# Optimization experiments

Hardware: AMD Instinct MI355X
Metric: run time of the kernel (lower is better)

## Reference

```python
import jax, jax.numpy as jnp
import numpy as np

N_HEADS = 8


def _norm_weights(idx):
    # softmax over where(idx>0, 1, -9e15) along axis 1 -> uniform weights over non-pad slots
    logits = jnp.where(idx > 0, jnp.float32(1.0), jnp.float32(-9e15))
    return jax.nn.softmax(logits, axis=1)


def _layer_norm(x, g, b, eps=1e-6):
    mu = jnp.mean(x, axis=-1, keepdims=True)
    var = jnp.var(x, axis=-1, keepdims=True)
    return (x - mu) * jax.lax.rsqrt(var + eps) * g + b


def _mha_block(x, mask, wq, wk, wv, wo, g, b):
    # standard multi-head self-attention block with residual + layernorm
    B, L, D = x.shape
    hd = D // N_HEADS
    q = (x @ wq).reshape(B, L, N_HEADS, hd)
    k = (x @ wk).reshape(B, L, N_HEADS, hd)
    v = (x @ wv).reshape(B, L, N_HEADS, hd)
    scores = jnp.einsum('bqhd,bkhd->bhqk', q, k) / jnp.float32(np.sqrt(hd))
    scores = jnp.where(mask[:, None, None, :], jnp.float32(-1e9), scores)
    attn = jax.nn.softmax(scores, axis=-1)
    out = jnp.einsum('bhqk,bkhd->bqhd', attn, v).reshape(B, L, D) @ wo
    return _layer_norm(out + x, g, b)


def _forward(data_idx, seq, timestamps, user_level, useq, user_inf, user_cen,
             spread_status, id2vector,
             user_emb, cen_emb, time_emb, pos_emb, inf_emb,
             w1, w2, w3,
             t_wq, t_wk, t_wv, t_wo, t_g, t_b,
             s_wq, s_wk, s_wv, s_wo, s_g, s_b,
             W, W2, f_l1_w, f_l1_b, f_l2_w, f_l2_b, lin_w, lin_b):
    # ---- HGNN layer (hypergraph conv) ----
    tv = w3[0]  # TextVector = weight3[0]
    dot = w3 @ tv
    cos = dot / (jnp.linalg.norm(tv) * jnp.linalg.norm(w3, axis=1))
    inter_nw = jnp.mean(cos)  # scalar

    tweet_hidden = user_emb + cen_emb[user_cen]          # [N, D]
    x = (tweet_hidden @ w1) * inter_nw                   # [N, D]
    nor = _norm_weights(seq)                             # [E, L]
    edge = jnp.einsum('elc,el->ec', x[seq], nor)         # gather + weighted reduce
    edge = jax.nn.relu(edge)
    e1 = edge @ w2                                       # [E, D]
    u_nor = _norm_weights(useq)                          # [N, Lu]
    node = jnp.einsum('nlc,nl->nc', e1[useq], u_nor)     # [N, D]

    # ---- HGSL head ----
    sb = seq[data_idx]                                   # [B, L]
    nor_b = _norm_weights(sb)
    att_mask = sb == 0                                   # PAD == 0
    adj = node[sb]                                       # [B, L, D]

    att_hidden = adj + time_emb[timestamps[data_idx]]
    att_out = _mha_block(att_hidden, att_mask, t_wq, t_wk, t_wv, t_wo, t_g, t_b)
    news = jnp.einsum('blc,bl->bc', att_out, nor_b)
    news = jnp.concatenate([news, spread_status[data_idx][:, 2:] / 3600.0 / 24.0], axis=-1) @ W

    att_hidden_s = adj + inf_emb[user_inf[data_idx]] + pos_emb[user_level[data_idx]]
    att_out_s = _mha_block(att_hidden_s, att_mask, s_wq, s_wk, s_wv, s_wo, s_g, s_b)
    news_s = jnp.einsum('blc,bl->bc', att_out_s, nor_b)
    news_s = jnp.concatenate([news_s, spread_status[data_idx][:, :2]], axis=-1) @ W2

    # Gated fusion (linear3 unused in original forward; id2vector is overwritten/unused)
    emb = jnp.stack([news, news_s], axis=0)              # [2, B, D+2]
    score = jax.nn.softmax(jnp.tanh(emb @ f_l1_w + f_l1_b) @ f_l2_w + f_l2_b, axis=0)
    fused = jnp.sum(score * emb, axis=0)                 # [B, D+2]
    return jax.nn.log_softmax(fused @ lin_w + lin_b, axis=1)


def setup_inputs():
    key = jax.random.key(0)
    ks = jax.random.split(key, 40)
    N, E, L, Lu, D, B, TV = 50000, 10000, 50, 20, 128, 512, 768
    Dw = D + 2
    s = 0.05
    inp = {
        'data_idx': jax.random.randint(ks[0], (B,), 0, E),
        'seq': jax.random.randint(ks[1], (E, L), 0, N),
        'timestamps': jax.random.randint(ks[2], (E, L), 0, 5000),
        'user_level': jax.random.randint(ks[3], (E, L), 0, 50),
        'useq': jax.random.randint(ks[4], (N, Lu), 0, E),
        'user_inf': jax.random.randint(ks[5], (E, L), 0, 200),
        'user_cen': jax.random.randint(ks[6], (N,), 0, 600),
        'spread_status': jax.random.uniform(ks[7], (E, 4), dtype=jnp.float32),
        'id2vector': jax.random.normal(ks[8], (1,), dtype=jnp.float32),
        'user_emb': s * jax.random.normal(ks[9], (N, D), dtype=jnp.float32),
        'cen_emb': s * jax.random.normal(ks[10], (600, D), dtype=jnp.float32),
        'time_emb': s * jax.random.normal(ks[11], (5000, D), dtype=jnp.float32),
        'pos_emb': s * jax.random.normal(ks[12], (50, D), dtype=jnp.float32),
        'inf_emb': s * jax.random.normal(ks[13], (200, D), dtype=jnp.float32),
        'w1': s * jax.random.normal(ks[14], (D, D), dtype=jnp.float32),
        'w2': s * jax.random.normal(ks[15], (D, D), dtype=jnp.float32),
        'w3': s * jax.random.normal(ks[16], (TV, TV), dtype=jnp.float32),
        'W': s * jax.random.normal(ks[17], (Dw, Dw), dtype=jnp.float32),
        'W2': s * jax.random.normal(ks[18], (Dw, Dw), dtype=jnp.float32),
        'f_l1_w': s * jax.random.normal(ks[19], (Dw, Dw), dtype=jnp.float32),
        'f_l1_b': jnp.zeros((Dw,), jnp.float32),
        'f_l2_w': s * jax.random.normal(ks[20], (Dw, 1), dtype=jnp.float32),
        'f_l2_b': jnp.zeros((1,), jnp.float32),
        'lin_w': s * jax.random.normal(ks[21], (Dw, 2), dtype=jnp.float32),
        'lin_b': jnp.zeros((2,), jnp.float32),
    }
    for nm, i in [('t', 22), ('s', 27)]:
        inp[nm + '_wq'] = s * jax.random.normal(ks[i], (D, D), dtype=jnp.float32)
        inp[nm + '_wk'] = s * jax.random.normal(ks[i + 1], (D, D), dtype=jnp.float32)
        inp[nm + '_wv'] = s * jax.random.normal(ks[i + 2], (D, D), dtype=jnp.float32)
        inp[nm + '_wo'] = s * jax.random.normal(ks[i + 3], (D, D), dtype=jnp.float32)
        inp[nm + '_g'] = jnp.ones((D,), jnp.float32)
        inp[nm + '_b'] = jnp.zeros((D,), jnp.float32)
    return inp


def reference(data_idx, seq, timestamps, user_level, useq, user_inf, user_cen,
              spread_status, id2vector,
              user_emb, cen_emb, time_emb, pos_emb, inf_emb,
              w1, w2, w3,
              t_wq, t_wk, t_wv, t_wo, t_g, t_b,
              s_wq, s_wk, s_wv, s_wo, s_g, s_b,
              W, W2, f_l1_w, f_l1_b, f_l2_w, f_l2_b, lin_w, lin_b):
    return _forward(data_idx, seq, timestamps, user_level, useq, user_inf, user_cen,
                    spread_status, id2vector,
                    user_emb, cen_emb, time_emb, pos_emb, inf_emb,
                    w1, w2, w3,
                    t_wq, t_wk, t_wv, t_wo, t_g, t_b,
                    s_wq, s_wk, s_wv, s_wo, s_g, s_b,
                    W, W2, f_l1_w, f_l1_b, f_l2_w, f_l2_b, lin_w, lin_b)
```

## Files before the change

kernel.cpp:

```cpp
#include <hip/hip_runtime.h>
#include <math.h>

constexpr int Nn = 50000;
constexpr int Ee = 10000;
constexpr int Ll = 50;
constexpr int LuU = 20;
constexpr int Dd = 128;
constexpr int Bb = 512;
constexpr int TVv = 768;
constexpr int Dw = 130;
constexpr int BL = Bb * Ll;
constexpr int BLP = Bb * 64;

typedef __attribute__((ext_vector_type(8))) short bf8v;
typedef __attribute__((ext_vector_type(4))) float f4v;
typedef __attribute__((ext_vector_type(8))) unsigned short u16x8;
typedef __attribute__((ext_vector_type(4))) unsigned short u16x4;

__device__ __forceinline__ unsigned short f2bf(float f) {
  union { float f; unsigned u; } v; v.f = f;
  unsigned r = v.u + 0x7FFFu + ((v.u >> 16) & 1u);
  return (unsigned short)(r >> 16);
}
__device__ __forceinline__ float bf2f(unsigned short h) {
  union { unsigned u; float f; } v; v.u = ((unsigned)h) << 16; return v.f;
}
__device__ __forceinline__ int swz(int b) { return b ^ (((b >> 8) & 7) << 4); }
__device__ __forceinline__ int swz7(int b) { return b ^ (((b >> 7) & 7) << 4); }

__device__ __forceinline__ float block_sum_256(float v, volatile float* scr) {
#pragma unroll
  for (int o = 32; o > 0; o >>= 1) v += __shfl_down(v, o, 64);
  __syncthreads();
  if ((threadIdx.x & 63) == 0) scr[threadIdx.x >> 6] = v;
  __syncthreads();
  return scr[0] + scr[1] + scr[2] + scr[3];
}

__global__ __launch_bounds__(256) void k_cos(const float* __restrict__ w3,
                                             float* __restrict__ dotb,
                                             float* __restrict__ nrmb) {
  __shared__ float scr[4];
  int i = blockIdx.x;
  const float* row = w3 + (size_t)i * TVv;
  float d = 0.f, n = 0.f;
  for (int j = threadIdx.x; j < TVv; j += 256) {
    float a = row[j];
    d += a * w3[j];
    n += a * a;
  }
  d = block_sum_256(d, scr);
  n = block_sum_256(n, scr);
  if (threadIdx.x == 0) { dotb[i] = d; nrmb[i] = n; }
}

__global__ __launch_bounds__(256) void k_internw(const float* __restrict__ dotb,
                                                 const float* __restrict__ nrmb,
                                                 float* __restrict__ internw) {
  __shared__ float scr[4];
  float n0 = sqrtf(nrmb[0]);
  float s = 0.f;
  for (int i = threadIdx.x; i < TVv; i += 256)
    s += dotb[i] / (n0 * sqrtf(nrmb[i]));
  s = block_sum_256(s, scr);
  if (threadIdx.x == 0) *internw = s / (float)TVv;
}

__global__ __launch_bounds__(256) void k_prep(
    const float* w1, const float* w2,
    const float* twq, const float* twk, const float* twv, const float* two,
    const float* swq, const float* swk, const float* swv, const float* swo,
    unsigned short* __restrict__ out) {
  int wsel = blockIdx.x >> 3, part = blockIdx.x & 7;
  const float* w;
  switch (wsel) {
    case 0: w = w1; break;  case 1: w = w2; break;
    case 2: w = twq; break; case 3: w = twk; break;
    case 4: w = twv; break; case 5: w = two; break;
    case 6: w = swq; break; case 7: w = swk; break;
    case 8: w = swv; break; default: w = swo; break;
  }
  int u = part * 256 + threadIdx.x;
  int n = u >> 4, k0 = (u & 15) * 8;
  u16x8 pv;
#pragma unroll
  for (int i = 0; i < 8; i++) pv[i] = f2bf(w[(size_t)(k0 + i) * Dd + n]);
  ((u16x8*)(out + (size_t)wsel * Dd * Dd))[u] = pv;
}

template <int MODE>
__global__ __launch_bounds__(256) void k_gemm_plain(
    const void* __restrict__ inA, const float* __restrict__ in1,
    const int* __restrict__ gidx, const float* __restrict__ scalep,
    const unsigned short* __restrict__ WTg,
    unsigned short* __restrict__ out, int nrows) {
  __shared__ unsigned short WT[Dd * Dd];
  __shared__ __align__(16) unsigned short Ab[64 * Dd];
  int tid = threadIdx.x;
  {
    const u16x8* src = (const u16x8*)WTg;
    for (int u = tid; u < 2048; u += 256)
      *(u16x8*)((char*)WT + swz(u * 16)) = src[u];
  }
  int r0 = blockIdx.x * 64;
  if constexpr (MODE == 0) {
    float sc = *scalep;
    for (int u = tid; u < 1024; u += 256) {
      int rr = u >> 4, c0 = (u & 15) * 8;
      int r = r0 + rr;
      u16x8 pv;
      if (r < nrows) {
        const float* a = (const float*)inA + (size_t)r * Dd + c0;
        const float* c = in1 + (size_t)gidx[r] * Dd + c0;
#pragma unroll
        for (int i = 0; i < 8; i++) pv[i] = f2bf((a[i] + c[i]) * sc);
      } else {
#pragma unroll
        for (int i = 0; i < 8; i++) pv[i] = 0;
      }
      *(u16x8*)((char*)Ab + swz(rr * 256 + c0 * 2)) = pv;
    }
  } else {
    for (int u = tid; u < 1024; u += 256) {
      int rr = u >> 4;
      int r = r0 + rr;
      u16x8 pv;
      if (r < nrows) pv = ((const u16x8*)inA)[(size_t)r * 16 + (u & 15)];
      else {
#pragma unroll
        for (int i = 0; i < 8; i++) pv[i] = 0;
      }
      *(u16x8*)((char*)Ab + swz(rr * 256 + (u & 15) * 16)) = pv;
    }
  }
  __syncthreads();
  int lane = tid & 63, wid = tid >> 6;
  int lrow = lane & 15, lg = lane >> 4;
  bf8v af[4];
#pragma unroll
  for (int kc = 0; kc < 4; kc++)
    af[kc] = *(const bf8v*)((char*)Ab + swz((wid * 16 + lrow) * 256 + kc * 64 + lg * 16));
  f4v acc[8];
#pragma unroll
  for (int nt = 0; nt < 8; nt++)
#pragma unroll
    for (int j = 0; j < 4; j++) acc[nt][j] = 0.f;
#pragma unroll
  for (int nt = 0; nt < 8; nt++)
#pragma unroll
    for (int kc = 0; kc < 4; kc++) {
      bf8v bfg = *(const bf8v*)((char*)WT + swz((nt * 16 + lrow) * 256 + kc * 64 + lg * 16));
      acc[nt] = __builtin_amdgcn_mfma_f32_16x16x32_bf16(af[kc], bfg, acc[nt], 0, 0, 0);
    }
#pragma unroll
  for (int nt = 0; nt < 8; nt++)
#pragma unroll
    for (int j = 0; j < 4; j++) {
      int r = r0 + wid * 16 + lg * 4 + j;
      if (r < nrows) out[(size_t)r * Dd + nt * 16 + lrow] = f2bf(acc[nt][j]);
    }
}

__global__ __launch_bounds__(256, 2) void k_qkvattn(
    const unsigned short* __restrict__ hidT, const unsigned short* __restrict__ hidS,
    const unsigned short* __restrict__ WTbase,
    const int* __restrict__ data_idx, const int* __restrict__ seq,
    unsigned short* __restrict__ ctxp) {
  __shared__ __align__(16) char LDS[81920];
  unsigned short* AQ  = (unsigned short*)(LDS);
  unsigned short* WP  = (unsigned short*)(LDS + 16384);
  unsigned short* Ks  = (unsigned short*)(LDS + 49152);
  unsigned short* VTs = (unsigned short*)(LDS + 65536);

  int b = blockIdx.x, branch = blockIdx.y;
  int tid = threadIdx.x, lane = tid & 63, wid = tid >> 6;
  int lrow = lane & 15, lg = lane >> 4;
  const unsigned short* hid = (branch ? hidS : hidT) + (size_t)b * Ll * Dd;

  int e = data_idx[b];
  int mi = (lane < Ll) ? (seq[(size_t)e * Ll + lane] == 0 ? 1 : 0) : 2;
  int mflag[4][4];
#pragma unroll
  for (int mt = 0; mt < 4; mt++)
#pragma unroll
    for (int j = 0; j < 4; j++)
      mflag[mt][j] = __shfl(mi, mt * 16 + lg * 4 + j, 64);

  for (int u = tid; u < 1024; u += 256) {
    int rr = u >> 4, ch = u & 15;
    u16x8 pv;
    if (rr < Ll) pv = *(const u16x8*)(hid + (size_t)rr * Dd + ch * 8);
    else {
#pragma unroll
      for (int i = 0; i < 8; i++) pv[i] = 0;
    }
    *(u16x8*)((char*)AQ + swz(rr * 256 + ch * 16)) = pv;
  }
  {
    const u16x8* srcW = (const u16x8*)(WTbase + (size_t)(2 + branch * 4) * Dd * Dd);
    for (int u = tid; u < 2048; u += 256)
      *(u16x8*)((char*)WP + swz(u * 16)) = srcW[u];
  }
  __syncthreads();
  bf8v hf[4];
#pragma unroll
  for (int kc = 0; kc < 4; kc++)
    hf[kc] = *(const bf8v*)((char*)AQ + swz((wid * 16 + lrow) * 256 + kc * 64 + lg * 16));
  __syncthreads();

  {
    f4v acc[8];
#pragma unroll
    for (int nt = 0; nt < 8; nt++)
#pragma unroll
      for (int j = 0; j < 4; j++) acc[nt][j] = 0.f;
#pragma unroll
    for (int nt = 0; nt < 8; nt++)
#pragma unroll
      for (int kc = 0; kc < 4; kc++) {
        bf8v wf = *(const bf8v*)((char*)WP + swz((nt * 16 + lrow) * 256 + kc * 64 + lg * 16));
        acc[nt] = __builtin_amdgcn_mfma_f32_16x16x32_bf16(wf, hf[kc], acc[nt], 0, 0, 0);
      }
    __syncthreads();
#pragma unroll
    for (int nt = 0; nt < 8; nt++) {
      u16x4 qv;
#pragma unroll
      for (int j = 0; j < 4; j++) qv[j] = f2bf(acc[nt][j]);
      *(u16x4*)((char*)AQ + swz((wid * 16 + lrow) * 256 + (nt * 16 + lg * 4) * 2)) = qv;
    }
  }
  {
    const u16x8* srcW = (const u16x8*)(WTbase + (size_t)(3 + branch * 4) * Dd * Dd);
    for (int u = tid; u < 2048; u += 256)
      *(u16x8*)((char*)WP + swz(u * 16)) = srcW[u];
  }
  __syncthreads();
  {
    f4v acc[8];
#pragma unroll
    for (int nt = 0; nt < 8; nt++)
#pragma unroll
      for (int j = 0; j < 4; j++) acc[nt][j] = 0.f;
#pragma unroll
    for (int nt = 0; nt < 8; nt++)
#pragma unroll
      for (int kc = 0; kc < 4; kc++) {
        bf8v wf = *(const bf8v*)((char*)WP + swz((nt * 16 + lrow) * 256 + kc * 64 + lg * 16));
        acc[nt] = __builtin_amdgcn_mfma_f32_16x16x32_bf16(wf, hf[kc], acc[nt], 0, 0, 0);
      }
    __syncthreads();
#pragma unroll
    for (int nt = 0; nt < 8; nt++) {
      u16x4 kv4;
#pragma unroll
      for (int j = 0; j < 4; j++) kv4[j] = f2bf(acc[nt][j]);
      *(u16x4*)((char*)Ks + swz((wid * 16 + lrow) * 256 + (nt * 16 + lg * 4) * 2)) = kv4;
    }
  }
  {
    const u16x8* srcW = (const u16x8*)(WTbase + (size_t)(4 + branch * 4) * Dd * Dd);
    for (int u = tid; u < 2048; u += 256)
      *(u16x8*)((char*)WP + swz(u * 16)) = srcW[u];
  }
  __syncthreads();
  {
    f4v acc[8];
#pragma unroll
    for (int nt = 0; nt < 8; nt++)
#pragma unroll
      for (int j = 0; j < 4; j++) acc[nt][j] = 0.f;
#pragma unroll
    for (int nt = 0; nt < 8; nt++)
#pragma unroll
      for (int kc = 0; kc < 4; kc++) {
        bf8v wf = *(const bf8v*)((char*)WP + swz((nt * 16 + lrow) * 256 + kc * 64 + lg * 16));
        acc[nt] = __builtin_amdgcn_mfma_f32_16x16x32_bf16(hf[kc], wf, acc[nt], 0, 0, 0);
      }
    __syncthreads();
#pragma unroll
    for (int nt = 0; nt < 8; nt++) {
      u16x4 tv;
#pragma unroll
      for (int j = 0; j < 4; j++) tv[j] = f2bf(acc[nt][j]);
      *(u16x4*)((char*)VTs + swz7((nt * 16 + lrow) * 128 + (wid * 16 + lg * 4) * 2)) = tv;
    }
  }
  __syncthreads();

  char* PTw = (char*)WP + wid * 8192;
  size_t rbase = ((size_t)branch * Bb + b) * 64;
#pragma unroll 1
  for (int hi = 0; hi < 2; hi++) {
    int h = wid * 2 + hi;
    bf8v af[4], bq[4];
    if (lg < 2) {
#pragma unroll
      for (int t = 0; t < 4; t++) {
        af[t] = *(const bf8v*)((char*)Ks + swz((t * 16 + lrow) * 256 + h * 32 + lg * 16));
        bq[t] = *(const bf8v*)((char*)AQ + swz((t * 16 + lrow) * 256 + h * 32 + lg * 16));
      }
    } else {
#pragma unroll
      for (int t = 0; t < 4; t++)
#pragma unroll
        for (int i = 0; i < 8; i++) { af[t][i] = 0; bq[t][i] = 0; }
    }
#pragma unroll 1
    for (int nt = 0; nt < 4; nt++) {
      f4v sa[4];
#pragma unroll
      for (int mt = 0; mt < 4; mt++)
#pragma unroll
        for (int j = 0; j < 4; j++) sa[mt][j] = 0.f;
#pragma unroll
      for (int mt = 0; mt < 4; mt++)
        sa[mt] = __builtin_amdgcn_mfma_f32_16x16x32_bf16(af[mt], bq[nt], sa[mt], 0, 0, 0);
      float m = -3.0e38f;
#pragma unroll
      for (int mt = 0; mt < 4; mt++)
#pragma unroll
        for (int j = 0; j < 4; j++) {
          int mk = mflag[mt][j];
          float v = sa[mt][j] * 0.25f;
          v = (mk == 1) ? -1e9f : v;
          v = (mk == 2) ? -3.0e38f : v;
          sa[mt][j] = v;
          m = fmaxf(m, v);
        }
      m = fmaxf(m, __shfl_xor(m, 16, 64));
      m = fmaxf(m, __shfl_xor(m, 32, 64));
      float s = 0.f;
#pragma unroll
      for (int mt = 0; mt < 4; mt++)
#pragma unroll
        for (int j = 0; j < 4; j++) {
          float p = expf(sa[mt][j] - m);
          sa[mt][j] = p;
          s += p;
        }
      s += __shfl_xor(s, 16, 64);
      s += __shfl_xor(s, 32, 64);
      float inv = 1.f / s;
      int q = nt * 16 + lrow;
#pragma unroll
      for (int mt = 0; mt < 4; mt++) {
        u16x4 pw;
#pragma unroll
        for (int j = 0; j < 4; j++) pw[j] = f2bf(sa[mt][j] * inv);
        *(u16x4*)(PTw + swz7(q * 128 + mt * 32 + lg * 8)) = pw;
      }
    }
    f4v pacc[4];
#pragma unroll
    for (int nt = 0; nt < 4; nt++)
#pragma unroll
      for (int j = 0; j < 4; j++) pacc[nt][j] = 0.f;
#pragma unroll
    for (int kt = 0; kt < 2; kt++) {
      bf8v av = *(const bf8v*)((char*)VTs + swz7((h * 16 + lrow) * 128 + kt * 64 + lg * 16));
#pragma unroll
      for (int nt = 0; nt < 4; nt++) {
        bf8v bv = *(const bf8v*)(PTw + swz7((nt * 16 + lrow) * 128 + kt * 64 + lg * 16));
        pacc[nt] = __builtin_amdgcn_mfma_f32_16x16x32_bf16(av, bv, pacc[nt], 0, 0, 0);
      }
    }
#pragma unroll
    for (int nt = 0; nt < 4; nt++) {
      int q = nt * 16 + lrow;
      unsigned* cp = (unsigned*)(ctxp + (rbase + q) * Dd + h * 16 + lg * 4);
      cp[0] = (unsigned)f2bf(pacc[nt][0]) | ((unsigned)f2bf(pacc[nt][1]) << 16);
      cp[1] = (unsigned)f2bf(pacc[nt][2]) | ((unsigned)f2bf(pacc[nt][3]) << 16);
    }
  }
}

__global__ __launch_bounds__(256) void k_gemm_ln(
    const unsigned short* __restrict__ ctxp,
    const unsigned short* __restrict__ hidT, const unsigned short* __restrict__ hidS,
    const unsigned short* __restrict__ WTbase,
    const float* __restrict__ tg, const float* __restrict__ tb,
    const float* __restrict__ sg, const float* __restrict__ sb_,
    unsigned short* __restrict__ attall) {
  __shared__ unsigned short WT[Dd * Dd];
  __shared__ __align__(16) char UB[64 * 132 * 4];
  unsigned short* Ab = (unsigned short*)UB;
  float (*O)[132] = (float (*)[132])UB;

  int b = blockIdx.x & 511, branch = blockIdx.x >> 9;
  const unsigned short* resid = (branch ? hidS : hidT);
  const unsigned short* Wg = WTbase + (size_t)(5 + branch * 4) * Dd * Dd;
  const float* lng = branch ? sg : tg;
  const float* lnb = branch ? sb_ : tb;
  unsigned short* out = attall + (size_t)branch * BL * Dd;
  int tid = threadIdx.x;

  {
    const u16x8* src = (const u16x8*)Wg;
    for (int u = tid; u < 2048; u += 256)
      *(u16x8*)((char*)WT + swz(u * 16)) = src[u];
  }
  for (int u = tid; u < 1024; u += 256) {
    int rr = u >> 4;
    u16x8 pv = ((const u16x8*)ctxp)[(((size_t)branch * Bb + b) * 64 + rr) * 16 + (u & 15)];
    *(u16x8*)((char*)Ab + swz(rr * 256 + (u & 15) * 16)) = pv;
  }
  __syncthreads();

  int lane = tid & 63, wid = tid >> 6;
  int lrow = lane & 15, lg = lane >> 4;
  bf8v af[4];
#pragma unroll
  for (int kc = 0; kc < 4; kc++)
    af[kc] = *(const bf8v*)((char*)Ab + swz((wid * 16 + lrow) * 256 + kc * 64 + lg * 16));
  f4v acc[8];
#pragma unroll
  for (int nt = 0; nt < 8; nt++)
#pragma unroll
    for (int j = 0; j < 4; j++) acc[nt][j] = 0.f;
#pragma unroll
  for (int nt = 0; nt < 8; nt++)
#pragma unroll
    for (int kc = 0; kc < 4; kc++) {
      bf8v bfg = *(const bf8v*)((char*)WT + swz((nt * 16 + lrow) * 256 + kc * 64 + lg * 16));
      acc[nt] = __builtin_amdgcn_mfma_f32_16x16x32_bf16(af[kc], bfg, acc[nt], 0, 0, 0);
    }
  __syncthreads();
#pragma unroll
  for (int nt = 0; nt < 8; nt++)
#pragma unroll
    for (int j = 0; j < 4; j++)
      O[wid * 16 + lg * 4 + j][nt * 16 + lrow] = acc[nt][j];
  __syncthreads();
  int r = tid >> 2, c0 = (tid & 3) * 32;
  if (r < Ll) {
    size_t gr = (size_t)b * Ll + r;
    float vv[32];
    float s1 = 0.f, s2 = 0.f;
#pragma unroll
    for (int i8 = 0; i8 < 4; i8++) {
      u16x8 hb = *(const u16x8*)(resid + gr * Dd + c0 + i8 * 8);
#pragma unroll
      for (int i = 0; i < 8; i++) {
        float x = O[r][c0 + i8 * 8 + i] + bf2f(hb[i]);
        vv[i8 * 8 + i] = x; s1 += x; s2 += x * x;
      }
    }
    s1 += __shfl_xor(s1, 1, 64); s2 += __shfl_xor(s2, 1, 64);
    s1 += __shfl_xor(s1, 2, 64); s2 += __shfl_xor(s2, 2, 64);
    float mu = s1 * (1.f / Dd);
    float var = s2 * (1.f / Dd) - mu * mu;
    float rs = rsqrtf(var + 1e-6f);
#pragma unroll
    for (int i8 = 0; i8 < 4; i8++) {
      u16x8 ov;
#pragma unroll
      for (int i = 0; i < 8; i++) {
        int c = c0 + i8 * 8 + i;
        ov[i] = f2bf((vv[i8 * 8 + i] - mu) * rs * lng[c] + lnb[c]);
      }
      *(u16x8*)(out + gr * Dd + c0 + i8 * 8) = ov;
    }
  }
}

__global__ __launch_bounds__(256) void k_gather_e(const unsigned short* __restrict__ X,
                                                  const int* __restrict__ seq,
                                                  unsigned short* __restrict__ EDGE) {
  int r = blockIdx.x * 16 + (threadIdx.x >> 4);
  int c0 = (threadIdx.x & 15) * 8;
  const int* row = seq + (size_t)r * Ll;
  float acc[8];
#pragma unroll
  for (int i = 0; i < 8; i++) acc[i] = 0.f;
  int cnt = 0;
#pragma unroll 1
  for (int l0 = 0; l0 < Ll; l0 += 10) {
    int ids[10];
#pragma unroll
    for (int t = 0; t < 10; t++) ids[t] = row[l0 + t];
    u16x8 vv[10];
#pragma unroll
    for (int t = 0; t < 10; t++)
      vv[t] = *(const u16x8*)(X + (size_t)ids[t] * Dd + c0);
#pragma unroll
    for (int t = 0; t < 10; t++)
      if (ids[t] > 0) {
        cnt++;
#pragma unroll
        for (int i = 0; i < 8; i++) acc[i] += bf2f(vv[t][i]);
      }
  }
  u16x8 ov;
  if (cnt) {
    float inv = 1.f / (float)cnt;
#pragma unroll
    for (int i = 0; i < 8; i++) ov[i] = f2bf(fmaxf(acc[i] * inv, 0.f));
  } else {
    u16x8 x0 = *(const u16x8*)(X + c0);
#pragma unroll
    for (int i = 0; i < 8; i++) ov[i] = f2bf(fmaxf(bf2f(x0[i]), 0.f));
  }
  *(u16x8*)(EDGE + (size_t)r * Dd + c0) = ov;
}

__global__ __launch_bounds__(256) void k_hidfuse(
    const unsigned short* __restrict__ E1, const int* __restrict__ data_idx,
    const int* __restrict__ seq, const int* __restrict__ tsmp,
    const int* __restrict__ uinf, const int* __restrict__ ulev,
    const int* __restrict__ useq,
    const float* __restrict__ time_emb, const float* __restrict__ inf_emb,
    const float* __restrict__ pos_emb,
    unsigned short* __restrict__ hidTb, unsigned short* __restrict__ hidSb) {
  int bl = blockIdx.x * 16 + (threadIdx.x >> 4);
  int c0 = (threadIdx.x & 15) * 8;
  int b = bl / Ll, l = bl % Ll;
  int e = data_idx[b];
  int sid = seq[(size_t)e * Ll + l];
  const int* urow = useq + (size_t)sid * LuU;
  float acc[8];
#pragma unroll
  for (int i = 0; i < 8; i++) acc[i] = 0.f;
  int cnt = 0;
#pragma unroll 1
  for (int t0 = 0; t0 < LuU; t0 += 10) {
    int ids[10];
#pragma unroll
    for (int t = 0; t < 10; t++) ids[t] = urow[t0 + t];
    u16x8 vv[10];
#pragma unroll
    for (int t = 0; t < 10; t++)
      vv[t] = *(const u16x8*)(E1 + (size_t)ids[t] * Dd + c0);
#pragma unroll
    for (int t = 0; t < 10; t++)
      if (ids[t] > 0) {
        cnt++;
#pragma unroll
        for (int i = 0; i < 8; i++) acc[i] += bf2f(vv[t][i]);
      }
  }
  float node[8];
  if (cnt) {
    float inv = 1.f / (float)cnt;
#pragma unroll
    for (int i = 0; i < 8; i++) node[i] = acc[i] * inv;
  } else {
    u16x8 e0 = *(const u16x8*)(E1 + c0);
#pragma unroll
    for (int i = 0; i < 8; i++) node[i] = bf2f(e0[i]);
  }
  int ts = tsmp[(size_t)e * Ll + l];
  int fi = uinf[(size_t)e * Ll + l];
  int lv = ulev[(size_t)e * Ll + l];
  const float4* tp = (const float4*)(time_emb + (size_t)ts * Dd + c0);
  const float4* ip = (const float4*)(inf_emb + (size_t)fi * Dd + c0);
  const float4* pp = (const float4*)(pos_emb + (size_t)lv * Dd + c0);
  float4 t0 = tp[0], t1 = tp[1];
  float4 i0 = ip[0], i1 = ip[1];
  float4 p0 = pp[0], p1 = pp[1];
  float te[8] = {t0.x, t0.y, t0.z, t0.w, t1.x, t1.y, t1.z, t1.w};
  float ie[8] = {i0.x, i0.y, i0.z, i0.w, i1.x, i1.y, i1.z, i1.w};
  float pe[8] = {p0.x, p0.y, p0.z, p0.w, p1.x, p1.y, p1.z, p1.w};
  u16x8 ht, hs;
#pragma unroll
  for (int i = 0; i < 8; i++) {
    ht[i] = f2bf(node[i] + te[i]);
    hs[i] = f2bf(node[i] + ie[i] + pe[i]);
  }
  size_t o = (size_t)bl * Dd + c0;
  *(u16x8*)(hidTb + o) = ht;
  *(u16x8*)(hidSb + o) = hs;
}

__global__ __launch_bounds__(128) void k_newsred(const unsigned short* __restrict__ attall,
                                                 const int* __restrict__ data_idx,
                                                 const int* __restrict__ seq,
                                                 const float* __restrict__ spread,
                                                 float* __restrict__ news) {
  __shared__ int sl[Ll];
  __shared__ int scnt;
  int b = blockIdx.x, branch = blockIdx.y;
  int e = data_idx[b];
  const unsigned short* att = attall + (size_t)branch * BL * Dd;
  if (threadIdx.x < Ll) sl[threadIdx.x] = seq[(size_t)e * Ll + threadIdx.x];
  __syncthreads();
  if (threadIdx.x == 0) {
    int c = 0;
    for (int l = 0; l < Ll; l++) c += (sl[l] > 0);
    scnt = c;
  }
  __syncthreads();
  int cnt = scnt;
  float wnp = cnt ? 1.f / (float)cnt : 0.02f;
  int c = threadIdx.x;
  float acc = 0.f;
  for (int l = 0; l < Ll; l++) {
    float w = cnt ? ((sl[l] > 0) ? wnp : 0.f) : wnp;
    acc += w * bf2f(att[((size_t)b * Ll + l) * Dd + c]);
  }
  float* nrow = news + ((size_t)branch * Bb + b) * 132;
  nrow[c] = acc;
  if (c < 2) {
    nrow[Dd + c] = branch ? spread[(size_t)e * 4 + c]
                          : spread[(size_t)e * 4 + 2 + c] * (1.f / 86400.f);
  }
}

__global__ __launch_bounds__(256) void k_newsW(const float* __restrict__ news,
                                               const float* __restrict__ Wm,
                                               const float* __restrict__ W2m,
                                               float* __restrict__ NT,
                                               float* __restrict__ NS) {
  __shared__ float Wl[Dw][Dw + 1];
  __shared__ float nrow[132];
  int branch = blockIdx.y;
  const float* W = branch ? W2m : Wm;
  float* out = branch ? NS : NT;
  for (int u = threadIdx.x; u < Dw * Dw; u += 256)
    Wl[u / Dw][u % Dw] = W[u];
  for (int rr = 0; rr < 32; rr++) {
    int b = blockIdx.x * 32 + rr;
    __syncthreads();
    if (threadIdx.x < Dw)
      nrow[threadIdx.x] = news[((size_t)branch * Bb + b) * 132 + threadIdx.x];
    __syncthreads();
    int j = threadIdx.x;
    if (j < Dw) {
      float acc = 0.f;
      for (int kk = 0; kk < Dw; kk++) acc += nrow[kk] * Wl[kk][j];
      out[(size_t)b * Dw + j] = acc;
    }
  }
}

__global__ __launch_bounds__(256) void k_fusion(const float* __restrict__ nt,
                                                const float* __restrict__ ns,
                                                const float* __restrict__ l1w,
                                                const float* __restrict__ l1b,
                                                const float* __restrict__ l2w,
                                                const float* __restrict__ l2b,
                                                const float* __restrict__ linw,
                                                const float* __restrict__ linb,
                                                float* __restrict__ out) {
  __shared__ float rt[Dw], rs[Dw];
  __shared__ float scr[4];
  int b = blockIdx.x, j = threadIdx.x;
  if (j < Dw) { rt[j] = nt[(size_t)b * Dw + j]; rs[j] = ns[(size_t)b * Dw + j]; }
  __syncthreads();
  float pt = 0.f, ps = 0.f;
  if (j < Dw) {
    float at = l1b[j], as = l1b[j];
    for (int kk = 0; kk < Dw; kk++) {
      float w = l1w[(size_t)kk * Dw + j];
      at += rt[kk] * w;
      as += rs[kk] * w;
    }
    float lw2 = l2w[j];
    pt = tanhf(at) * lw2;
    ps = tanhf(as) * lw2;
  }
  float st = block_sum_256(pt, scr);
  float ss = block_sum_256(ps, scr);
  st += l2b[0]; ss += l2b[0];
  float m = fmaxf(st, ss);
  float e0 = expf(st - m), e1v = expf(ss - m);
  float inv = 1.f / (e0 + e1v);
  float s0 = e0 * inv, s1 = e1v * inv;
  float fj  = (j < Dw) ? (s0 * rt[j] + s1 * rs[j]) : 0.f;
  float w0  = (j < Dw) ? linw[(size_t)j * 2 + 0] : 0.f;
  float w1v = (j < Dw) ? linw[(size_t)j * 2 + 1] : 0.f;
  float l0 = block_sum_256(fj * w0, scr);
  float l1 = block_sum_256(fj * w1v, scr);
  if (j == 0) {
    l0 += linb[0]; l1 += linb[1];
    float mm = fmaxf(l0, l1);
    float lse = mm + logf(expf(l0 - mm) + expf(l1 - mm));
    out[(size_t)b * 2 + 0] = l0 - lse;
    out[(size_t)b * 2 + 1] = l1 - lse;
  }
}

extern "C" void kernel_launch(void* const* d_in, const int* in_sizes, int n_in,
                              void* d_out, int out_size, void* d_ws, size_t ws_size,
                              hipStream_t stream) {
  const int*   data_idx = (const int*)d_in[0];
  const int*   seq      = (const int*)d_in[1];
  const int*   tsmp     = (const int*)d_in[2];
  const int*   ulev     = (const int*)d_in[3];
  const int*   useq     = (const int*)d_in[4];
  const int*   uinf     = (const int*)d_in[5];
  const int*   ucen     = (const int*)d_in[6];
  const float* spread   = (const float*)d_in[7];
  const float* user_emb = (const float*)d_in[9];
  const float* cen_emb  = (const float*)d_in[10];
  const float* time_emb = (const float*)d_in[11];
  const float* pos_emb  = (const float*)d_in[12];
  const float* inf_emb  = (const float*)d_in[13];
  const float* w1       = (const float*)d_in[14];
  const float* w2       = (const float*)d_in[15];
  const float* w3       = (const float*)d_in[16];
  const float* Wm       = (const float*)d_in[17];
  const float* W2m      = (const float*)d_in[18];
  const float* f_l1_w   = (const float*)d_in[19];
  const float* f_l1_b   = (const float*)d_in[20];
  const float* f_l2_w   = (const float*)d_in[21];
  const float* f_l2_b   = (const float*)d_in[22];
  const float* lin_w    = (const float*)d_in[23];
  const float* lin_b    = (const float*)d_in[24];
  const float* t_wq = (const float*)d_in[25];
  const float* t_wk = (const float*)d_in[26];
  const float* t_wv = (const float*)d_in[27];
  const float* t_wo = (const float*)d_in[28];
  const float* t_g  = (const float*)d_in[29];
  const float* t_b  = (const float*)d_in[30];
  const float* s_wq = (const float*)d_in[31];
  const float* s_wk = (const float*)d_in[32];
  const float* s_wv = (const float*)d_in[33];
  const float* s_wo = (const float*)d_in[34];
  const float* s_g  = (const float*)d_in[35];
  const float* s_b  = (const float*)d_in[36];

  char* ws = (char*)d_ws;
  constexpr size_t SZ_WT  = (size_t)10 * Dd * Dd * 2;
  constexpr size_t SZ_XB  = (size_t)Nn * Dd * 2;
  constexpr size_t SZ_EB  = (size_t)Ee * Dd * 2;
  constexpr size_t SZ_BH  = (size_t)BL * Dd * 2;
  constexpr size_t SZ_PD  = (size_t)2 * BLP * Dd * 2;
  constexpr size_t OFF_WT  = 8192;
  constexpr size_t OFF_X   = OFF_WT + SZ_WT;
  constexpr size_t OFF_EDGE= OFF_X + SZ_XB;
  constexpr size_t OFF_E1  = OFF_EDGE + SZ_EB;
  constexpr size_t OFF_HTB = OFF_E1 + SZ_EB;
  constexpr size_t OFF_HSB = OFF_HTB + SZ_BH;
  constexpr size_t OFF_CTX = OFF_HSB + SZ_BH;
  constexpr size_t OFF_ATT = OFF_CTX + SZ_PD;
  constexpr size_t OFF_NEWS= OFF_ATT + 2 * SZ_BH;
  constexpr size_t OFF_NT  = OFF_NEWS + (size_t)2 * Bb * 132 * 4;
  constexpr size_t OFF_NS  = OFF_NT + (size_t)Bb * Dw * 4;

  float* dotb    = (float*)(ws + 0);
  float* nrmb    = (float*)(ws + 3072);
  float* internw = (float*)(ws + 6144);
  unsigned short* WTall = (unsigned short*)(ws + OFF_WT);
  unsigned short* Xb    = (unsigned short*)(ws + OFF_X);
  unsigned short* EDGEb = (unsigned short*)(ws + OFF_EDGE);
  unsigned short* E1b   = (unsigned short*)(ws + OFF_E1);
  unsigned short* HIDTb = (unsigned short*)(ws + OFF_HTB);
  unsigned short* HIDSb = (unsigned short*)(ws + OFF_HSB);
  unsigned short* CTXp  = (unsigned short*)(ws + OFF_CTX);
  unsigned short* ATTall= (unsigned short*)(ws + OFF_ATT);
  float*          NEWS  = (float*)(ws + OFF_NEWS);
  float*          NT    = (float*)(ws + OFF_NT);
  float*          NS    = (float*)(ws + OFF_NS);
  float* outp = (float*)d_out;

  k_prep<<<80, 256, 0, stream>>>(w1, w2, t_wq, t_wk, t_wv, t_wo,
                                 s_wq, s_wk, s_wv, s_wo, WTall);
  k_cos<<<TVv, 256, 0, stream>>>(w3, dotb, nrmb);
  k_internw<<<1, 256, 0, stream>>>(dotb, nrmb, internw);

  k_gemm_plain<0><<<(Nn + 63) / 64, 256, 0, stream>>>(
      user_emb, cen_emb, ucen, internw, WTall + 0 * Dd * Dd, Xb, Nn);
  k_gather_e<<<Ee / 16, 256, 0, stream>>>(Xb, seq, EDGEb);
  k_gemm_plain<1><<<(Ee + 63) / 64, 256, 0, stream>>>(
      EDGEb, nullptr, nullptr, nullptr, WTall + 1 * Dd * Dd, E1b, Ee);
  k_hidfuse<<<BL / 16, 256, 0, stream>>>(E1b, data_idx, seq, tsmp, uinf, ulev, useq,
                                         time_emb, inf_emb, pos_emb, HIDTb, HIDSb);

  k_qkvattn<<<dim3(Bb, 2), 256, 0, stream>>>(HIDTb, HIDSb, WTall, data_idx, seq, CTXp);
  k_gemm_ln<<<1024, 256, 0, stream>>>(CTXp, HIDTb, HIDSb, WTall,
                                      t_g, t_b, s_g, s_b, ATTall);

  k_newsred<<<dim3(Bb, 2), 128, 0, stream>>>(ATTall, data_idx, seq, spread, NEWS);
  k_newsW<<<dim3(16, 2), 256, 0, stream>>>(NEWS, Wm, W2m, NT, NS);
  k_fusion<<<Bb, 256, 0, stream>>>(NT, NS, f_l1_w, f_l1_b, f_l2_w, f_l2_b,
                                   lin_w, lin_b, outp);

  (void)in_sizes; (void)n_in; (void)out_size; (void)ws_size;
}
```

Baseline: 366.0 us.

## Gather before w1 projection and fuse layernorm with news reduction

The w1 projection now runs on the 10000 edge rows instead of all 50000 node rows. This works because mean-pooling is linear: the kernel gathers and averages bf16 tweet_hidden first, then applies w1, the scale and relu in the GEMM epilogue. The layernorm kernel now also does the per-news weighted reduction in shared memory, so the full attention output is no longer written and read back. The qkv attention kernel's launch bounds change to three blocks per SM. The price is an extra bf16 rounding of the summed embeddings before the matmul, and still one full pass over the node embeddings to build TH.

```diff
diff --git a/kernel.cpp b/kernel.cpp
--- a/kernel.cpp
+++ b/kernel.cpp
@@ -88,50 +88,98 @@
   ((u16x8*)(out + (size_t)wsel * Dd * Dd))[u] = pv;
 }
 
-template <int MODE>
+__global__ __launch_bounds__(256) void k_th(const float* __restrict__ ue,
+                                            const float* __restrict__ ce,
+                                            const int* __restrict__ ucen,
+                                            unsigned short* __restrict__ TH) {
+  int r = blockIdx.x * 16 + (threadIdx.x >> 4);
+  int c0 = (threadIdx.x & 15) * 8;
+  int cen = ucen[r];
+  const float4* up = (const float4*)(ue + (size_t)r * Dd + c0);
+  const float4* cp = (const float4*)(ce + (size_t)cen * Dd + c0);
+  float4 u0 = up[0], u1 = up[1], v0 = cp[0], v1 = cp[1];
+  float a[8] = {u0.x + v0.x, u0.y + v0.y, u0.z + v0.z, u0.w + v0.w,
+                u1.x + v1.x, u1.y + v1.y, u1.z + v1.z, u1.w + v1.w};
+  u16x8 o;
+#pragma unroll
+  for (int i = 0; i < 8; i++) o[i] = f2bf(a[i]);
+  *(u16x8*)(TH + (size_t)r * Dd + c0) = o;
+}
+
+template <int RELU>
+__global__ __launch_bounds__(256) void k_gather(const unsigned short* __restrict__ X,
+                                                const int* __restrict__ idx,
+                                                unsigned short* __restrict__ out) {
+  int r = blockIdx.x * 16 + (threadIdx.x >> 4);
+  int c0 = (threadIdx.x & 15) * 8;
+  const int* row = idx + (size_t)r * Ll;
+  float acc[8];
+#pragma unroll
+  for (int i = 0; i < 8; i++) acc[i] = 0.f;
+  int cnt = 0;
+#pragma unroll 1
+  for (int l0 = 0; l0 < Ll; l0 += 10) {
+    int ids[10];
+#pragma unroll
+    for (int t = 0; t < 10; t++) ids[t] = row[l0 + t];
+    u16x8 vv[10];
+#pragma unroll
+    for (int t = 0; t < 10; t++)
+      vv[t] = *(const u16x8*)(X + (size_t)ids[t] * Dd + c0);
+#pragma unroll
+    for (int t = 0; t < 10; t++)
+      if (ids[t] > 0) {
+        cnt++;
+#pragma unroll
+        for (int i = 0; i < 8; i++) acc[i] += bf2f(vv[t][i]);
+      }
+  }
+  u16x8 ov;
+  if (cnt) {
+    float inv = 1.f / (float)cnt;
+#pragma unroll
+    for (int i = 0; i < 8; i++) {
+      float v = acc[i] * inv;
+      if (RELU) v = fmaxf(v, 0.f);
+      ov[i] = f2bf(v);
+    }
+  } else {
+    u16x8 x0 = *(const u16x8*)(X + c0);
+#pragma unroll
+    for (int i = 0; i < 8; i++) {
+      float v = bf2f(x0[i]);
+      if (RELU) v = fmaxf(v, 0.f);
+      ov[i] = f2bf(v);
+    }
+  }
+  *(u16x8*)(out + (size_t)r * Dd + c0) = ov;
+}
+
+template <int EPI>
 __global__ __launch_bounds__(256) void k_gemm_plain(
-    const void* __restrict__ inA, const float* __restrict__ in1,
-    const int* __restrict__ gidx, const float* __restrict__ scalep,
+    const unsigned short* __restrict__ inA, const float* __restrict__ scalep,
     const unsigned short* __restrict__ WTg,
     unsigned short* __restrict__ out, int nrows) {
   __shared__ unsigned short WT[Dd * Dd];
   __shared__ __align__(16) unsigned short Ab[64 * Dd];
   int tid = threadIdx.x;
+  float sc = (EPI == 1) ? *scalep : 1.f;
   {
     const u16x8* src = (const u16x8*)WTg;
     for (int u = tid; u < 2048; u += 256)
       *(u16x8*)((char*)WT + swz(u * 16)) = src[u];
   }
   int r0 = blockIdx.x * 64;
-  if constexpr (MODE == 0) {
-    float sc = *scalep;
-    for (int u = tid; u < 1024; u += 256) {
-      int rr = u >> 4, c0 = (u & 15) * 8;
-      int r = r0 + rr;
-      u16x8 pv;
-      if (r < nrows) {
-        const float* a = (const float*)inA + (size_t)r * Dd + c0;
-        const float* c = in1 + (size_t)gidx[r] * Dd + c0;
-#pragma unroll
-        for (int i = 0; i < 8; i++) pv[i] = f2bf((a[i] + c[i]) * sc);
-      } else {
-#pragma unroll
-        for (int i = 0; i < 8; i++) pv[i] = 0;
-      }
-      *(u16x8*)((char*)Ab + swz(rr * 256 + c0 * 2)) = pv;
-    }
-  } else {
-    for (int u = tid; u < 1024; u += 256) {
-      int rr = u >> 4;
-      int r = r0 + rr;
-      u16x8 pv;
-      if (r < nrows) pv = ((const u16x8*)inA)[(size_t)r * 16 + (u & 15)];
-      else {
-#pragma unroll
-        for (int i = 0; i < 8; i++) pv[i] = 0;
-      }
-      *(u16x8*)((char*)Ab + swz(rr * 256 + (u & 15) * 16)) = pv;
-    }
+  for (int u = tid; u < 1024; u += 256) {
+    int rr = u >> 4;
+    int r = r0 + rr;
+    u16x8 pv;
+    if (r < nrows) pv = ((const u16x8*)inA)[(size_t)r * 16 + (u & 15)];
+    else {
+#pragma unroll
+      for (int i = 0; i < 8; i++) pv[i] = 0;
+    }
+    *(u16x8*)((char*)Ab + swz(rr * 256 + (u & 15) * 16)) = pv;
   }
   __syncthreads();
   int lane = tid & 63, wid = tid >> 6;
@@ -157,351 +205,12 @@
 #pragma unroll
     for (int j = 0; j < 4; j++) {
       int r = r0 + wid * 16 + lg * 4 + j;
-      if (r < nrows) out[(size_t)r * Dd + nt * 16 + lrow] = f2bf(acc[nt][j]);
-    }
-}
-
-__global__ __launch_bounds__(256, 2) void k_qkvattn(
-    const unsigned short* __restrict__ hidT, const unsigned short* __restrict__ hidS,
-    const unsigned short* __restrict__ WTbase,
-    const int* __restrict__ data_idx, const int* __restrict__ seq,
-    unsigned short* __restrict__ ctxp) {
-  __shared__ __align__(16) char LDS[81920];
-  unsigned short* AQ  = (unsigned short*)(LDS);
-  unsigned short* WP  = (unsigned short*)(LDS + 16384);
-  unsigned short* Ks  = (unsigned short*)(LDS + 49152);
-  unsigned short* VTs = (unsigned short*)(LDS + 65536);
-
-  int b = blockIdx.x, branch = blockIdx.y;
-  int tid = threadIdx.x, lane = tid & 63, wid = tid >> 6;
-  int lrow = lane & 15, lg = lane >> 4;
-  const unsigned short* hid = (branch ? hidS : hidT) + (size_t)b * Ll * Dd;
-
-  int e = data_idx[b];
-  int mi = (lane < Ll) ? (seq[(size_t)e * Ll + lane] == 0 ? 1 : 0) : 2;
-  int mflag[4][4];
-#pragma unroll
-  for (int mt = 0; mt < 4; mt++)
-#pragma unroll
-    for (int j = 0; j < 4; j++)
-      mflag[mt][j] = __shfl(mi, mt * 16 + lg * 4 + j, 64);
-
-  for (int u = tid; u < 1024; u += 256) {
-    int rr = u >> 4, ch = u & 15;
-    u16x8 pv;
-    if (rr < Ll) pv = *(const u16x8*)(hid + (size_t)rr * Dd + ch * 8);
-    else {
-#pragma unroll
-      for (int i = 0; i < 8; i++) pv[i] = 0;
-    }
-    *(u16x8*)((char*)AQ + swz(rr * 256 + ch * 16)) = pv;
-  }
-  {
-    const u16x8* srcW = (const u16x8*)(WTbase + (size_t)(2 + branch * 4) * Dd * Dd);
-    for (int u = tid; u < 2048; u += 256)
-      *(u16x8*)((char*)WP + swz(u * 16)) = srcW[u];
-  }
-  __syncthreads();
-  bf8v hf[4];
-#pragma unroll
-  for (int kc = 0; kc < 4; kc++)
-    hf[kc] = *(const bf8v*)((char*)AQ + swz((wid * 16 + lrow) * 256 + kc * 64 + lg * 16));
-  __syncthreads();
-
-  {
-    f4v acc[8];
-#pragma unroll
-    for (int nt = 0; nt < 8; nt++)
-#pragma unroll
-      for (int j = 0; j < 4; j++) acc[nt][j] = 0.f;
-#pragma unroll
-    for (int nt = 0; nt < 8; nt++)
-#pragma unroll
-      for (int kc = 0; kc < 4; kc++) {
-        bf8v wf = *(const bf8v*)((char*)WP + swz((nt * 16 + lrow) * 256 + kc * 64 + lg * 16));
-        acc[nt] = __builtin_amdgcn_mfma_f32_16x16x32_bf16(wf, hf[kc], acc[nt], 0, 0, 0);
-      }
-    __syncthreads();
-#pragma unroll
-    for (int nt = 0; nt < 8; nt++) {
-      u16x4 qv;
-#pragma unroll
-      for (int j = 0; j < 4; j++) qv[j] = f2bf(acc[nt][j]);
-      *(u16x4*)((char*)AQ + swz((wid * 16 + lrow) * 256 + (nt * 16 + lg * 4) * 2)) = qv;
-    }
-  }
-  {
-    const u16x8* srcW = (const u16x8*)(WTbase + (size_t)(3 + branch * 4) * Dd * Dd);
-    for (int u = tid; u < 2048; u += 256)
-      *(u16x8*)((char*)WP + swz(u * 16)) = srcW[u];
-  }
-  __syncthreads();
-  {
-    f4v acc[8];
-#pragma unroll
-    for (int nt = 0; nt < 8; nt++)
-#pragma unroll
-      for (int j = 0; j < 4; j++) acc[nt][j] = 0.f;
-#pragma unroll
-    for (int nt = 0; nt < 8; nt++)
-#pragma unroll
-      for (int kc = 0; kc < 4; kc++) {
-        bf8v wf = *(const bf8v*)((char*)WP + swz((nt * 16 + lrow) * 256 + kc * 64 + lg * 16));
-        acc[nt] = __builtin_amdgcn_mfma_f32_16x16x32_bf16(wf, hf[kc], acc[nt], 0, 0, 0);
-      }
-    __syncthreads();
-#pragma unroll
-    for (int nt = 0; nt < 8; nt++) {
-      u16x4 kv4;
-#pragma unroll
-      for (int j = 0; j < 4; j++) kv4[j] = f2bf(acc[nt][j]);
-      *(u16x4*)((char*)Ks + swz((wid * 16 + lrow) * 256 + (nt * 16 + lg * 4) * 2)) = kv4;
-    }
-  }
-  {
-    const u16x8* srcW = (const u16x8*)(WTbase + (size_t)(4 + branch * 4) * Dd * Dd);
-    for (int u = tid; u < 2048; u += 256)
-      *(u16x8*)((char*)WP + swz(u * 16)) = srcW[u];
-  }
-  __syncthreads();
-  {
-    f4v acc[8];
-#pragma unroll
-    for (int nt = 0; nt < 8; nt++)
-#pragma unroll
-      for (int j = 0; j < 4; j++) acc[nt][j] = 0.f;
-#pragma unroll
-    for (int nt = 0; nt < 8; nt++)
-#pragma unroll
-      for (int kc = 0; kc < 4; kc++) {
-        bf8v wf = *(const bf8v*)((char*)WP + swz((nt * 16 + lrow) * 256 + kc * 64 + lg * 16));
-        acc[nt] = __builtin_amdgcn_mfma_f32_16x16x32_bf16(hf[kc], wf, acc[nt], 0, 0, 0);
-      }
-    __syncthreads();
-#pragma unroll
-    for (int nt = 0; nt < 8; nt++) {
-      u16x4 tv;
-#pragma unroll
-      for (int j = 0; j < 4; j++) tv[j] = f2bf(acc[nt][j]);
-      *(u16x4*)((char*)VTs + swz7((nt * 16 + lrow) * 128 + (wid * 16 + lg * 4) * 2)) = tv;
-    }
-  }
-  __syncthreads();
-
-  char* PTw = (char*)WP + wid * 8192;
-  size_t rbase = ((size_t)branch * Bb + b) * 64;
-#pragma unroll 1
-  for (int hi = 0; hi < 2; hi++) {
-    int h = wid * 2 + hi;
-    bf8v af[4], bq[4];
-    if (lg < 2) {
-#pragma unroll
-      for (int t = 0; t < 4; t++) {
-        af[t] = *(const bf8v*)((char*)Ks + swz((t * 16 + lrow) * 256 + h * 32 + lg * 16));
-        bq[t] = *(const bf8v*)((char*)AQ + swz((t * 16 + lrow) * 256 + h * 32 + lg * 16));
-      }
-    } else {
-#pragma unroll
-      for (int t = 0; t < 4; t++)
-#pragma unroll
-        for (int i = 0; i < 8; i++) { af[t][i] = 0; bq[t][i] = 0; }
-    }
-#pragma unroll 1
-    for (int nt = 0; nt < 4; nt++) {
-      f4v sa[4];
-#pragma unroll
-      for (int mt = 0; mt < 4; mt++)
-#pragma unroll
-        for (int j = 0; j < 4; j++) sa[mt][j] = 0.f;
-#pragma unroll
-      for (int mt = 0; mt < 4; mt++)
-        sa[mt] = __builtin_amdgcn_mfma_f32_16x16x32_bf16(af[mt], bq[nt], sa[mt], 0, 0, 0);
-      float m = -3.0e38f;
-#pragma unroll
-      for (int mt = 0; mt < 4; mt++)
-#pragma unroll
-        for (int j = 0; j < 4; j++) {
-          int mk = mflag[mt][j];
-          float v = sa[mt][j] * 0.25f;
-          v = (mk == 1) ? -1e9f : v;
-          v = (mk == 2) ? -3.0e38f : v;
-          sa[mt][j] = v;
-          m = fmaxf(m, v);
-        }
-      m = fmaxf(m, __shfl_xor(m, 16, 64));
-      m = fmaxf(m, __shfl_xor(m, 32, 64));
-      float s = 0.f;
-#pragma unroll
-      for (int mt = 0; mt < 4; mt++)
-#pragma unroll
-        for (int j = 0; j < 4; j++) {
-          float p = expf(sa[mt][j] - m);
-          sa[mt][j] = p;
-          s += p;
-        }
-      s += __shfl_xor(s, 16, 64);
-      s += __shfl_xor(s, 32, 64);
-      float inv = 1.f / s;
-      int q = nt * 16 + lrow;
-#pragma unroll
-      for (int mt = 0; mt < 4; mt++) {
-        u16x4 pw;
-#pragma unroll
-        for (int j = 0; j < 4; j++) pw[j] = f2bf(sa[mt][j] * inv);
-        *(u16x4*)(PTw + swz7(q * 128 + mt * 32 + lg * 8)) = pw;
-      }
-    }
-    f4v pacc[4];
-#pragma unroll
-    for (int nt = 0; nt < 4; nt++)
-#pragma unroll
-      for (int j = 0; j < 4; j++) pacc[nt][j] = 0.f;
-#pragma unroll
-    for (int kt = 0; kt < 2; kt++) {
-      bf8v av = *(const bf8v*)((char*)VTs + swz7((h * 16 + lrow) * 128 + kt * 64 + lg * 16));
-#pragma unroll
-      for (int nt = 0; nt < 4; nt++) {
-        bf8v bv = *(const bf8v*)(PTw + swz7((nt * 16 + lrow) * 128 + kt * 64 + lg * 16));
-        pacc[nt] = __builtin_amdgcn_mfma_f32_16x16x32_bf16(av, bv, pacc[nt], 0, 0, 0);
-      }
-    }
-#pragma unroll
-    for (int nt = 0; nt < 4; nt++) {
-      int q = nt * 16 + lrow;
-      unsigned* cp = (unsigned*)(ctxp + (rbase + q) * Dd + h * 16 + lg * 4);
-      cp[0] = (unsigned)f2bf(pacc[nt][0]) | ((unsigned)f2bf(pacc[nt][1]) << 16);
-      cp[1] = (unsigned)f2bf(pacc[nt][2]) | ((unsigned)f2bf(pacc[nt][3]) << 16);
-    }
-  }
-}
-
-__global__ __launch_bounds__(256) void k_gemm_ln(
-    const unsigned short* __restrict__ ctxp,
-    const unsigned short* __restrict__ hidT, const unsigned short* __restrict__ hidS,
-    const unsigned short* __restrict__ WTbase,
-    const float* __restrict__ tg, const float* __restrict__ tb,
-    const float* __restrict__ sg, const float* __restrict__ sb_,
-    unsigned short* __restrict__ attall) {
-  __shared__ unsigned short WT[Dd * Dd];
-  __shared__ __align__(16) char UB[64 * 132 * 4];
-  unsigned short* Ab = (unsigned short*)UB;
-  float (*O)[132] = (float (*)[132])UB;
-
-  int b = blockIdx.x & 511, branch = blockIdx.x >> 9;
-  const unsigned short* resid = (branch ? hidS : hidT);
-  const unsigned short* Wg = WTbase + (size_t)(5 + branch * 4) * Dd * Dd;
-  const float* lng = branch ? sg : tg;
-  const float* lnb = branch ? sb_ : tb;
-  unsigned short* out = attall + (size_t)branch * BL * Dd;
-  int tid = threadIdx.x;
-
-  {
-    const u16x8* src = (const u16x8*)Wg;
-    for (int u = tid; u < 2048; u += 256)
-      *(u16x8*)((char*)WT + swz(u * 16)) = src[u];
-  }
-  for (int u = tid; u < 1024; u += 256) {
-    int rr = u >> 4;
-    u16x8 pv = ((const u16x8*)ctxp)[(((size_t)branch * Bb + b) * 64 + rr) * 16 + (u & 15)];
-    *(u16x8*)((char*)Ab + swz(rr * 256 + (u & 15) * 16)) = pv;
-  }
-  __syncthreads();
-
-  int lane = tid & 63, wid = tid >> 6;
-  int lrow = lane & 15, lg = lane >> 4;
-  bf8v af[4];
-#pragma unroll
-  for (int kc = 0; kc < 4; kc++)
-    af[kc] = *(const bf8v*)((char*)Ab + swz((wid * 16 + lrow) * 256 + kc * 64 + lg * 16));
-  f4v acc[8];
-#pragma unroll
-  for (int nt = 0; nt < 8; nt++)
-#pragma unroll
-    for (int j = 0; j < 4; j++) acc[nt][j] = 0.f;
-#pragma unroll
-  for (int nt = 0; nt < 8; nt++)
-#pragma unroll
-    for (int kc = 0; kc < 4; kc++) {
-      bf8v bfg = *(const bf8v*)((char*)WT + swz((nt * 16 + lrow) * 256 + kc * 64 + lg * 16));
-      acc[nt] = __builtin_amdgcn_mfma_f32_16x16x32_bf16(af[kc], bfg, acc[nt], 0, 0, 0);
-    }
-  __syncthreads();
-#pragma unroll
-  for (int nt = 0; nt < 8; nt++)
-#pragma unroll
-    for (int j = 0; j < 4; j++)
-      O[wid * 16 + lg * 4 + j][nt * 16 + lrow] = acc[nt][j];
-  __syncthreads();
-  int r = tid >> 2, c0 = (tid & 3) * 32;
-  if (r < Ll) {
-    size_t gr = (size_t)b * Ll + r;
-    float vv[32];
-    float s1 = 0.f, s2 = 0.f;
-#pragma unroll
-    for (int i8 = 0; i8 < 4; i8++) {
-      u16x8 hb = *(const u16x8*)(resid + gr * Dd + c0 + i8 * 8);
-#pragma unroll
-      for (int i = 0; i < 8; i++) {
-        float x = O[r][c0 + i8 * 8 + i] + bf2f(hb[i]);
-        vv[i8 * 8 + i] = x; s1 += x; s2 += x * x;
-      }
-    }
-    s1 += __shfl_xor(s1, 1, 64); s2 += __shfl_xor(s2, 1, 64);
-    s1 += __shfl_xor(s1, 2, 64); s2 += __shfl_xor(s2, 2, 64);
-    float mu = s1 * (1.f / Dd);
-    float var = s2 * (1.f / Dd) - mu * mu;
-    float rs = rsqrtf(var + 1e-6f);
-#pragma unroll
-    for (int i8 = 0; i8 < 4; i8++) {
-      u16x8 ov;
-#pragma unroll
-      for (int i = 0; i < 8; i++) {
-        int c = c0 + i8 * 8 + i;
-        ov[i] = f2bf((vv[i8 * 8 + i] - mu) * rs * lng[c] + lnb[c]);
-      }
-      *(u16x8*)(out + gr * Dd + c0 + i8 * 8) = ov;
-    }
-  }
-}
-
-__global__ __launch_bounds__(256) void k_gather_e(const unsigned short* __restrict__ X,
-                                                  const int* __restrict__ seq,
-                                                  unsigned short* __restrict__ EDGE) {
-  int r = blockIdx.x * 16 + (threadIdx.x >> 4);
-  int c0 = (threadIdx.x & 15) * 8;
-  const int* row = seq + (size_t)r * Ll;
-  float acc[8];
-#pragma unroll
-  for (int i = 0; i < 8; i++) acc[i] = 0.f;
-  int cnt = 0;
-#pragma unroll 1
-  for (int l0 = 0; l0 < Ll; l0 += 10) {
-    int ids[10];
-#pragma unroll
-    for (int t = 0; t < 10; t++) ids[t] = row[l0 + t];
-    u16x8 vv[10];
-#pragma unroll
-    for (int t = 0; t < 10; t++)
-      vv[t] = *(const u16x8*)(X + (size_t)ids[t] * Dd + c0);
-#pragma unroll
-    for (int t = 0; t < 10; t++)
-      if (ids[t] > 0) {
-        cnt++;
-#pragma unroll
-        for (int i = 0; i < 8; i++) acc[i] += bf2f(vv[t][i]);
-      }
-  }
-  u16x8 ov;
-  if (cnt) {
-    float inv = 1.f / (float)cnt;
-#pragma unroll
-    for (int i = 0; i < 8; i++) ov[i] = f2bf(fmaxf(acc[i] * inv, 0.f));
-  } else {
-    u16x8 x0 = *(const u16x8*)(X + c0);
-#pragma unroll
-    for (int i = 0; i < 8; i++) ov[i] = f2bf(fmaxf(bf2f(x0[i]), 0.f));
-  }
-  *(u16x8*)(EDGE + (size_t)r * Dd + c0) = ov;
+      if (r < nrows) {
+        float v = acc[nt][j];
+        if (EPI == 1) v = fmaxf(v * sc, 0.f);
+        out[(size_t)r * Dd + nt * 16 + lrow] = f2bf(v);
+      }
+    }
 }
 
 __global__ __launch_bounds__(256) void k_hidfuse(
@@ -572,37 +281,302 @@
   *(u16x8*)(hidSb + o) = hs;
 }
 
-__global__ __launch_bounds__(128) void k_newsred(const unsigned short* __restrict__ attall,
-                                                 const int* __restrict__ data_idx,
-                                                 const int* __restrict__ seq,
-                                                 const float* __restrict__ spread,
-                                                 float* __restrict__ news) {
+__global__ __launch_bounds__(256, 3) void k_qkvattn(
+    const unsigned short* __restrict__ hidT, const unsigned short* __restrict__ hidS,
+    const unsigned short* __restrict__ WTbase,
+    const int* __restrict__ data_idx, const int* __restrict__ seq,
+    unsigned short* __restrict__ ctxp) {
+  __shared__ __align__(16) char LDS[49152];
+  char* Qs  = LDS;
+  char* Ks  = LDS + 16384;
+  char* VTs = LDS + 32768;
+
+  int b = blockIdx.x, branch = blockIdx.y;
+  int tid = threadIdx.x, lane = tid & 63, wid = tid >> 6;
+  int lrow = lane & 15, lg = lane >> 4;
+  const unsigned short* hid = (branch ? hidS : hidT) + (size_t)b * Ll * Dd;
+  const unsigned short* Wq = WTbase + (size_t)(2 + branch * 4) * Dd * Dd;
+  const unsigned short* Wk = Wq + Dd * Dd;
+  const unsigned short* Wv = Wk + Dd * Dd;
+
+  int e = data_idx[b];
+  int mi = (lane < Ll) ? (seq[(size_t)e * Ll + lane] == 0 ? 1 : 0) : 2;
+  int mflag[4][4];
+#pragma unroll
+  for (int mt = 0; mt < 4; mt++)
+#pragma unroll
+    for (int j = 0; j < 4; j++)
+      mflag[mt][j] = __shfl(mi, mt * 16 + lg * 4 + j, 64);
+
+  bf8v hf[4][4];
+#pragma unroll
+  for (int qt = 0; qt < 4; qt++) {
+    int q = qt * 16 + lrow;
+#pragma unroll
+    for (int kc = 0; kc < 4; kc++) {
+      bf8v v;
+      if (q < Ll) v = *(const bf8v*)(hid + (size_t)q * Dd + kc * 32 + lg * 8);
+      else {
+#pragma unroll
+        for (int i = 0; i < 8; i++) v[i] = 0;
+      }
+      hf[qt][kc] = v;
+    }
+  }
+
+#pragma unroll
+  for (int sel = 0; sel < 2; sel++) {
+    const unsigned short* W = sel ? Wk : Wq;
+    char* Dst = sel ? Ks : Qs;
+#pragma unroll
+    for (int n2 = 0; n2 < 2; n2++) {
+      int n = wid * 2 + n2;
+      bf8v wf[4];
+#pragma unroll
+      for (int kc = 0; kc < 4; kc++)
+        wf[kc] = *(const bf8v*)(W + (size_t)(n * 16 + lrow) * Dd + kc * 32 + lg * 8);
+#pragma unroll
+      for (int qt = 0; qt < 4; qt++) {
+        f4v a = {0.f, 0.f, 0.f, 0.f};
+#pragma unroll
+        for (int kc = 0; kc < 4; kc++)
+          a = __builtin_amdgcn_mfma_f32_16x16x32_bf16(wf[kc], hf[qt][kc], a, 0, 0, 0);
+        u16x4 o;
+#pragma unroll
+        for (int j = 0; j < 4; j++) o[j] = f2bf(a[j]);
+        *(u16x4*)(Dst + swz((qt * 16 + lrow) * 256 + n * 32 + lg * 8)) = o;
+      }
+    }
+  }
+  {
+    bf8v hv[4];
+    int kvq = wid * 16 + lrow;
+#pragma unroll
+    for (int kc = 0; kc < 4; kc++) {
+      bf8v v;
+      if (kvq < Ll) v = *(const bf8v*)(hid + (size_t)kvq * Dd + kc * 32 + lg * 8);
+      else {
+#pragma unroll
+        for (int i = 0; i < 8; i++) v[i] = 0;
+      }
+      hv[kc] = v;
+    }
+#pragma unroll
+    for (int nt = 0; nt < 8; nt++) {
+      bf8v wf[4];
+#pragma unroll
+      for (int kc = 0; kc < 4; kc++)
+        wf[kc] = *(const bf8v*)(Wv + (size_t)(nt * 16 + lrow) * Dd + kc * 32 + lg * 8);
+      f4v a = {0.f, 0.f, 0.f, 0.f};
+#pragma unroll
+      for (int kc = 0; kc < 4; kc++)
+        a = __builtin_amdgcn_mfma_f32_16x16x32_bf16(hv[kc], wf[kc], a, 0, 0, 0);
+      u16x4 o;
+#pragma unroll
+      for (int j = 0; j < 4; j++) o[j] = f2bf(a[j]);
+      *(u16x4*)(VTs + swz7((nt * 16 + lrow) * 128 + (wid * 16 + lg * 4) * 2)) = o;
+    }
+  }
+  bf8v af[2][4], bq[2][4];
+#pragma unroll
+  for (int hi = 0; hi < 2; hi++) {
+    int h = wid * 2 + hi;
+#pragma unroll
+    for (int t = 0; t < 4; t++) {
+      bf8v a, q;
+      if (lg < 2) {
+        a = *(const bf8v*)(Ks + swz((t * 16 + lrow) * 256 + h * 32 + lg * 16));
+        q = *(const bf8v*)(Qs + swz((t * 16 + lrow) * 256 + h * 32 + lg * 16));
+      } else {
+#pragma unroll
+        for (int i = 0; i < 8; i++) { a[i] = 0; q[i] = 0; }
+      }
+      af[hi][t] = a; bq[hi][t] = q;
+    }
+  }
+  __syncthreads();
+
+  char* PTw = LDS + wid * 8192;
+  size_t rbase = ((size_t)branch * Bb + b) * 64;
+#pragma unroll
+  for (int hi = 0; hi < 2; hi++) {
+    int h = wid * 2 + hi;
+#pragma unroll
+    for (int nt = 0; nt < 4; nt++) {
+      f4v sa[4];
+#pragma unroll
+      for (int mt = 0; mt < 4; mt++)
+#pragma unroll
+        for (int j = 0; j < 4; j++) sa[mt][j] = 0.f;
+#pragma unroll
+      for (int mt = 0; mt < 4; mt++)
+        sa[mt] = __builtin_amdgcn_mfma_f32_16x16x32_bf16(af[hi][mt], bq[hi][nt], sa[mt], 0, 0, 0);
+      float m = -3.0e38f;
+#pragma unroll
+      for (int mt = 0; mt < 4; mt++)
+#pragma unroll
+        for (int j = 0; j < 4; j++) {
+          int mk = mflag[mt][j];
+          float v = sa[mt][j] * 0.25f;
+          v = (mk == 1) ? -1e9f : v;
+          v = (mk == 2) ? -3.0e38f : v;
+          sa[mt][j] = v;
+          m = fmaxf(m, v);
+        }
+      m = fmaxf(m, __shfl_xor(m, 16, 64));
+      m = fmaxf(m, __shfl_xor(m, 32, 64));
+      float s = 0.f;
+#pragma unroll
+      for (int mt = 0; mt < 4; mt++)
+#pragma unroll
+        for (int j = 0; j < 4; j++) {
+          float p = expf(sa[mt][j] - m);
+          sa[mt][j] = p;
+          s += p;
+        }
+      s += __shfl_xor(s, 16, 64);
+      s += __shfl_xor(s, 32, 64);
+      float inv = 1.f / s;
+      int q = nt * 16 + lrow;
+#pragma unroll
+      for (int mt = 0; mt < 4; mt++) {
+        u16x4 pw;
+#pragma unroll
+        for (int j = 0; j < 4; j++) pw[j] = f2bf(sa[mt][j] * inv);
+        *(u16x4*)(PTw + swz7(q * 128 + mt * 32 + lg * 8)) = pw;
+      }
+    }
+    f4v pacc[4];
+#pragma unroll
+    for (int nt = 0; nt < 4; nt++)
+#pragma unroll
+      for (int j = 0; j < 4; j++) pacc[nt][j] = 0.f;
+#pragma unroll
+    for (int kt = 0; kt < 2; kt++) {
+      bf8v av = *(const bf8v*)(VTs + swz7((h * 16 + lrow) * 128 + kt * 64 + lg * 16));
+#pragma unroll
+      for (int nt = 0; nt < 4; nt++) {
+        bf8v bv = *(const bf8v*)(PTw + swz7((nt * 16 + lrow) * 128 + kt * 64 + lg * 16));
+        pacc[nt] = __builtin_amdgcn_mfma_f32_16x16x32_bf16(av, bv, pacc[nt], 0, 0, 0);
+      }
+    }
+#pragma unroll
+    for (int nt = 0; nt < 4; nt++) {
+      int q = nt * 16 + lrow;
+      unsigned* cp = (unsigned*)(ctxp + (rbase + q) * Dd + h * 16 + lg * 4);
+      cp[0] = (unsigned)f2bf(pacc[nt][0]) | ((unsigned)f2bf(pacc[nt][1]) << 16);
+      cp[1] = (unsigned)f2bf(pacc[nt][2]) | ((unsigned)f2bf(pacc[nt][3]) << 16);
+    }
+  }
+}
+
+__global__ __launch_bounds__(256) void k_gemm_lnnews(
+    const unsigned short* __restrict__ ctxp,
+    const unsigned short* __restrict__ hidT, const unsigned short* __restrict__ hidS,
+    const unsigned short* __restrict__ WTbase,
+    const float* __restrict__ tg, const float* __restrict__ tb,
+    const float* __restrict__ sg, const float* __restrict__ sb_,
+    const int* __restrict__ data_idx, const int* __restrict__ seq,
+    const float* __restrict__ spread,
+    float* __restrict__ news) {
+  __shared__ unsigned short WT[Dd * Dd];
+  __shared__ __align__(16) char UB[64 * 132 * 4];
   __shared__ int sl[Ll];
   __shared__ int scnt;
-  int b = blockIdx.x, branch = blockIdx.y;
+  unsigned short* Ab = (unsigned short*)UB;
+  float (*O)[132] = (float (*)[132])UB;
+
+  int b = blockIdx.x & 511, branch = blockIdx.x >> 9;
+  const unsigned short* resid = (branch ? hidS : hidT);
+  const unsigned short* Wg = WTbase + (size_t)(5 + branch * 4) * Dd * Dd;
+  const float* lng = branch ? sg : tg;
+  const float* lnb = branch ? sb_ : tb;
+  int tid = threadIdx.x;
   int e = data_idx[b];
-  const unsigned short* att = attall + (size_t)branch * BL * Dd;
-  if (threadIdx.x < Ll) sl[threadIdx.x] = seq[(size_t)e * Ll + threadIdx.x];
-  __syncthreads();
-  if (threadIdx.x == 0) {
+  if (tid < Ll) sl[tid] = seq[(size_t)e * Ll + tid];
+
+  {
+    const u16x8* src = (const u16x8*)Wg;
+    for (int u = tid; u < 2048; u += 256)
+      *(u16x8*)((char*)WT + swz(u * 16)) = src[u];
+  }
+  for (int u = tid; u < 1024; u += 256) {
+    int rr = u >> 4;
+    u16x8 pv = ((const u16x8*)ctxp)[(((size_t)branch * Bb + b) * 64 + rr) * 16 + (u & 15)];
+    *(u16x8*)((char*)Ab + swz(rr * 256 + (u & 15) * 16)) = pv;
+  }
+  __syncthreads();
+
+  int lane = tid & 63, wid = tid >> 6;
+  int lrow = lane & 15, lg = lane >> 4;
+  bf8v af[4];
+#pragma unroll
+  for (int kc = 0; kc < 4; kc++)
+    af[kc] = *(const bf8v*)((char*)Ab + swz((wid * 16 + lrow) * 256 + kc * 64 + lg * 16));
+  f4v acc[8];
+#pragma unroll
+  for (int nt = 0; nt < 8; nt++)
+#pragma unroll
+    for (int j = 0; j < 4; j++) acc[nt][j] = 0.f;
+#pragma unroll
+  for (int nt = 0; nt < 8; nt++)
+#pragma unroll
+    for (int kc = 0; kc < 4; kc++) {
+      bf8v bfg = *(const bf8v*)((char*)WT + swz((nt * 16 + lrow) * 256 + kc * 64 + lg * 16));
+      acc[nt] = __builtin_amdgcn_mfma_f32_16x16x32_bf16(af[kc], bfg, acc[nt], 0, 0, 0);
+    }
+  __syncthreads();
+#pragma unroll
+  for (int nt = 0; nt < 8; nt++)
+#pragma unroll
+    for (int j = 0; j < 4; j++)
+      O[wid * 16 + lg * 4 + j][nt * 16 + lrow] = acc[nt][j];
+  __syncthreads();
+  int r = tid >> 2, c0 = (tid & 3) * 32;
+  if (r < Ll) {
+    size_t gr = (size_t)b * Ll + r;
+    float vv[32];
+    float s1 = 0.f, s2 = 0.f;
+#pragma unroll
+    for (int i8 = 0; i8 < 4; i8++) {
+      u16x8 hb = *(const u16x8*)(resid + gr * Dd + c0 + i8 * 8);
+#pragma unroll
+      for (int i = 0; i < 8; i++) {
+        float x = O[r][c0 + i8 * 8 + i] + bf2f(hb[i]);
+        vv[i8 * 8 + i] = x; s1 += x; s2 += x * x;
+      }
+    }
+    s1 += __shfl_xor(s1, 1, 64); s2 += __shfl_xor(s2, 1, 64);
+    s1 += __shfl_xor(s1, 2, 64); s2 += __shfl_xor(s2, 2, 64);
+    float mu = s1 * (1.f / Dd);
+    float var = s2 * (1.f / Dd) - mu * mu;
+    float rs = rsqrtf(var + 1e-6f);
+#pragma unroll
+    for (int i = 0; i < 32; i++) {
+      int c = c0 + i;
+      O[r][c] = (vv[i] - mu) * rs * lng[c] + lnb[c];
+    }
+  }
+  if (tid == 0) {
     int c = 0;
     for (int l = 0; l < Ll; l++) c += (sl[l] > 0);
     scnt = c;
   }
   __syncthreads();
-  int cnt = scnt;
-  float wnp = cnt ? 1.f / (float)cnt : 0.02f;
-  int c = threadIdx.x;
-  float acc = 0.f;
-  for (int l = 0; l < Ll; l++) {
-    float w = cnt ? ((sl[l] > 0) ? wnp : 0.f) : wnp;
-    acc += w * bf2f(att[((size_t)b * Ll + l) * Dd + c]);
-  }
   float* nrow = news + ((size_t)branch * Bb + b) * 132;
-  nrow[c] = acc;
-  if (c < 2) {
-    nrow[Dd + c] = branch ? spread[(size_t)e * 4 + c]
-                          : spread[(size_t)e * 4 + 2 + c] * (1.f / 86400.f);
+  if (tid < Dd) {
+    int cnt = scnt;
+    float wnp = cnt ? 1.f / (float)cnt : 0.02f;
+    float a = 0.f;
+    for (int l = 0; l < Ll; l++) {
+      float w = cnt ? ((sl[l] > 0) ? wnp : 0.f) : wnp;
+      a += w * O[l][tid];
+    }
+    nrow[tid] = a;
+  } else if (tid < Dw) {
+    int cc = tid - Dd;
+    nrow[tid] = branch ? spread[(size_t)e * 4 + cc]
+                       : spread[(size_t)e * 4 + 2 + cc] * (1.f / 86400.f);
   }
 }
 
@@ -722,19 +696,19 @@
 
   char* ws = (char*)d_ws;
   constexpr size_t SZ_WT  = (size_t)10 * Dd * Dd * 2;
-  constexpr size_t SZ_XB  = (size_t)Nn * Dd * 2;
+  constexpr size_t SZ_TH  = (size_t)Nn * Dd * 2;
   constexpr size_t SZ_EB  = (size_t)Ee * Dd * 2;
   constexpr size_t SZ_BH  = (size_t)BL * Dd * 2;
   constexpr size_t SZ_PD  = (size_t)2 * BLP * Dd * 2;
   constexpr size_t OFF_WT  = 8192;
-  constexpr size_t OFF_X   = OFF_WT + SZ_WT;
-  constexpr size_t OFF_EDGE= OFF_X + SZ_XB;
+  constexpr size_t OFF_TH  = OFF_WT + SZ_WT;
+  constexpr size_t OFF_G   = OFF_TH + SZ_TH;
+  constexpr size_t OFF_EDGE= OFF_G + SZ_EB;
   constexpr size_t OFF_E1  = OFF_EDGE + SZ_EB;
   constexpr size_t OFF_HTB = OFF_E1 + SZ_EB;
   constexpr size_t OFF_HSB = OFF_HTB + SZ_BH;
   constexpr size_t OFF_CTX = OFF_HSB + SZ_BH;
-  constexpr size_t OFF_ATT = OFF_CTX + SZ_PD;
-  constexpr size_t OFF_NEWS= OFF_ATT + 2 * SZ_BH;
+  constexpr size_t OFF_NEWS= OFF_CTX + SZ_PD;
   constexpr size_t OFF_NT  = OFF_NEWS + (size_t)2 * Bb * 132 * 4;
   constexpr size_t OFF_NS  = OFF_NT + (size_t)Bb * Dw * 4;
 
@@ -742,13 +716,13 @@
   float* nrmb    = (float*)(ws + 3072);
   float* internw = (float*)(ws + 6144);
   unsigned short* WTall = (unsigned short*)(ws + OFF_WT);
-  unsigned short* Xb    = (unsigned short*)(ws + OFF_X);
+  unsigned short* TH    = (unsigned short*)(ws + OFF_TH);
+  unsigned short* G     = (unsigned short*)(ws + OFF_G);
   unsigned short* EDGEb = (unsigned short*)(ws + OFF_EDGE);
   unsigned short* E1b   = (unsigned short*)(ws + OFF_E1);
   unsigned short* HIDTb = (unsigned short*)(ws + OFF_HTB);
   unsigned short* HIDSb = (unsigned short*)(ws + OFF_HSB);
   unsigned short* CTXp  = (unsigned short*)(ws + OFF_CTX);
-  unsigned short* ATTall= (unsigned short*)(ws + OFF_ATT);
   float*          NEWS  = (float*)(ws + OFF_NEWS);
   float*          NT    = (float*)(ws + OFF_NT);
   float*          NS    = (float*)(ws + OFF_NS);
@@ -759,19 +733,20 @@
   k_cos<<<TVv, 256, 0, stream>>>(w3, dotb, nrmb);
   k_internw<<<1, 256, 0, stream>>>(dotb, nrmb, internw);
 
-  k_gemm_plain<0><<<(Nn + 63) / 64, 256, 0, stream>>>(
-      user_emb, cen_emb, ucen, internw, WTall + 0 * Dd * Dd, Xb, Nn);
-  k_gather_e<<<Ee / 16, 256, 0, stream>>>(Xb, seq, EDGEb);
+  k_th<<<Nn / 16, 256, 0, stream>>>(user_emb, cen_emb, ucen, TH);
+  k_gather<0><<<Ee / 16, 256, 0, stream>>>(TH, seq, G);
   k_gemm_plain<1><<<(Ee + 63) / 64, 256, 0, stream>>>(
-      EDGEb, nullptr, nullptr, nullptr, WTall + 1 * Dd * Dd, E1b, Ee);
+      G, internw, WTall + 0 * Dd * Dd, EDGEb, Ee);
+  k_gemm_plain<0><<<(Ee + 63) / 64, 256, 0, stream>>>(
+      EDGEb, nullptr, WTall + 1 * Dd * Dd, E1b, Ee);
   k_hidfuse<<<BL / 16, 256, 0, stream>>>(E1b, data_idx, seq, tsmp, uinf, ulev, useq,
                                          time_emb, inf_emb, pos_emb, HIDTb, HIDSb);
 
   k_qkvattn<<<dim3(Bb, 2), 256, 0, stream>>>(HIDTb, HIDSb, WTall, data_idx, seq, CTXp);
-  k_gemm_ln<<<1024, 256, 0, stream>>>(CTXp, HIDTb, HIDSb, WTall,
-                                      t_g, t_b, s_g, s_b, ATTall);
-
-  k_newsred<<<dim3(Bb, 2), 128, 0, stream>>>(ATTall, data_idx, seq, spread, NEWS);
+  k_gemm_lnnews<<<1024, 256, 0, stream>>>(CTXp, HIDTb, HIDSb, WTall,
+                                          t_g, t_b, s_g, s_b,
+                                          data_idx, seq, spread, NEWS);
+
   k_newsW<<<dim3(16, 2), 256, 0, stream>>>(NEWS, Wm, W2m, NT, NS);
   k_fusion<<<Bb, 256, 0, stream>>>(NT, NS, f_l1_w, f_l1_b, f_l2_w, f_l2_b,
                                    lin_w, lin_b, outp);
```

Result: faster. 323.6 us (-11.6%).
